# Kernel tuning notes

Measured on AMD Instinct MI355X. Metric: run time of the kernel, lower is better.

Reference implementation:

```python
import jax, jax.numpy as jnp
import numpy as np

BEV = 100  # fixed 100x100 BEV grid from __init__


def _bev_grids():
    # x: arange(-25+0.125, 25, 0.5) -> 100 vals; z: arange(0.125, 50, 0.5) -> 100 vals
    x = jnp.arange(-25.0 + 0.125, 25.0, 0.5, dtype=jnp.float32)
    z = jnp.arange(0.125, 50.0, 0.5, dtype=jnp.float32)
    zz, xx = jnp.meshgrid(z, x, indexing='ij')           # [100,100]
    xz = xx / zz                                          # [100,100]
    yz = jnp.stack([-1.0 / zz, 0.5 / zz, 2.0 / zz], 0)    # [3,100,100], planes y=-1,0.5,2
    return xz, yz


def _grid_sample_bilinear(img, grid):
    """torch.nn.functional.grid_sample, mode='bilinear', padding_mode='zeros',
    align_corners=False. img [B,C,H,W], grid [B,Hg,Wg,2] in [-1,1] (u=x, v=y)."""
    B, C, H, W = img.shape
    x = ((grid[..., 0] + 1.0) * W - 1.0) * 0.5            # unnormalized pixel x
    y = ((grid[..., 1] + 1.0) * H - 1.0) * 0.5
    x0f = jnp.floor(x)
    y0f = jnp.floor(y)
    x0 = x0f.astype(jnp.int32)
    y0 = y0f.astype(jnp.int32)
    x1 = x0 + 1
    y1 = y0 + 1
    wx1 = x - x0f
    wx0 = 1.0 - wx1
    wy1 = y - y0f
    wy0 = 1.0 - wy1

    def corner(xi, yi, w):
        valid = ((xi >= 0) & (xi < W) & (yi >= 0) & (yi < H)).astype(img.dtype)
        xi_c = jnp.clip(xi, 0, W - 1)
        yi_c = jnp.clip(yi, 0, H - 1)
        # per-batch gather: [C,H,W] indexed by [Hg,Wg] -> [C,Hg,Wg]
        vals = jax.vmap(lambda im, yy, xx_: im[:, yy, xx_])(img, yi_c, xi_c)
        return vals * (w * valid)[:, None]                 # [B,C,Hg,Wg]

    return (corner(x0, y0, wx0 * wy0) + corner(x1, y0, wx1 * wy0)
            + corner(x0, y1, wx0 * wy1) + corner(x1, y1, wx1 * wy1))


def setup_inputs() -> dict:
    key = jax.random.key(0)
    k1, k2, k3, k4, k5 = jax.random.split(key, 5)
    B, C, H, W = 8, 512, 88, 176
    img_w, img_h = 704, 352
    img_feature = jax.random.normal(k1, (B, C, H, W), dtype=jnp.float32)
    # realistic pinhole intrinsics so many BEV cells project in-bounds
    fx = jax.random.uniform(k2, (B,), minval=450.0, maxval=650.0)
    fy = jax.random.uniform(k3, (B,), minval=450.0, maxval=650.0)
    cx = img_w / 2.0 + jax.random.uniform(k4, (B,), minval=-8.0, maxval=8.0)
    cy = img_h / 2.0 + jax.random.uniform(k5, (B,), minval=-8.0, maxval=8.0)
    intrinsic = (jnp.zeros((B, 3, 3), dtype=jnp.float32)
                 .at[:, 0, 0].set(fx).at[:, 1, 1].set(fy)
                 .at[:, 0, 2].set(cx).at[:, 1, 2].set(cy)
                 .at[:, 2, 2].set(1.0))
    return {"img_feature": img_feature, "intrinsic": intrinsic,
            "img_w": img_w, "img_h": img_h}


def reference(img_feature, intrinsic, img_w, img_h):
    xz, yz = _bev_grids()
    fx = intrinsic[:, 0, 0][:, None, None]
    cx = intrinsic[:, 0, 2][:, None, None]
    fy = intrinsic[:, 1, 1][:, None, None]
    cy = intrinsic[:, 1, 2][:, None, None]
    u = ((fx * xz[None] + cx) / img_w - 0.5) * 2.0        # [B,100,100], shared by all 3 planes
    acc = None
    for k in range(3):                                     # 3 fixed height planes
        v = ((fy * yz[k][None] + cy) / img_h - 0.5) * 2.0
        grid = jnp.stack((u, v), axis=3)                   # [B,100,100,2]
        s = _grid_sample_bilinear(img_feature, grid)       # [B,C,100,100]
        acc = s if acc is None else acc + s
    return acc / 3.0
```

## Files before the change

### kernel.cpp

```cpp
#include <hip/hip_runtime.h>

#define BEVN 100
#define NB 8
#define NC 512
#define FH 88
#define FW 176
#define HWSZ (FH * FW)
#define NG4  (HWSZ / 4)
#define NPAIR (BEVN * BEVN / 2)

__device__ __forceinline__ unsigned bf16rne(float f) {
    const unsigned b = __float_as_uint(f);
    return (b + 0x7fffu + ((b >> 16) & 1u)) >> 16;
}
__device__ __forceinline__ float lo16f(unsigned u) { return __uint_as_float(u << 16); }
__device__ __forceinline__ float hi16f(unsigned u) { return __uint_as_float(u & 0xffff0000u); }

__global__ __launch_bounds__(1024, 8)
void vt_kernel(const float* __restrict__ img,
               const float* __restrict__ intr,
               const int* __restrict__ p_imw,
               const int* __restrict__ p_imh,
               float* __restrict__ out)
{
    __shared__ unsigned lds[HWSZ];
    __shared__ float4   ytab[BEVN * 3];

    const int blk = blockIdx.x;
    const int b   = blk >> 8;
    const int c0  = (blk & 255) * 2;
    const int bc0 = b * NC + c0;
    const int tid = (int)threadIdx.x;

    {
        const float4* __restrict__ s0 = (const float4*)(img + (size_t)bc0 * HWSZ);
        const float4* __restrict__ s1 = s0 + NG4;
        uint4* l4 = (uint4*)lds;
        for (int idx = tid; idx < NG4; idx += 1024) {
            const float4 a  = s0[idx];
            const float4 bb = s1[idx];
            uint4 u;
            u.x = bf16rne(a.x) | (bf16rne(bb.x) << 16);
            u.y = bf16rne(a.y) | (bf16rne(bb.y) << 16);
            u.z = bf16rne(a.z) | (bf16rne(bb.z) << 16);
            u.w = bf16rne(a.w) | (bf16rne(bb.w) << 16);
            l4[idx] = u;
        }
    }

    const float fx  = intr[b * 9 + 0];
    const float cxv = intr[b * 9 + 2];
    const float fy  = intr[b * 9 + 4];
    const float cyv = intr[b * 9 + 5];
    const float wsc = (float)FW / (float)p_imw[0];
    const float hsc = (float)FH / (float)p_imh[0];

    if (tid < BEVN * 3) {
        const int   i  = tid / 3;
        const int   k  = tid - 3 * i;
        const float z  = 0.125f + 0.5f * (float)i;
        const float iz = 1.0f / z;
        const float yk = (k == 0) ? -1.0f : ((k == 1) ? 0.5f : 2.0f);
        const float yp = fmaf(fy * yk * iz + cyv, hsc, -0.5f);
        const float yf = floorf(yp);
        const int   y0 = (int)yf;
        float wy1 = yp - yf;
        float wy0 = 1.0f - wy1;
        wy0 = ((unsigned)y0 < (unsigned)FH) ? wy0 : 0.0f;
        wy1 = ((unsigned)(y0 + 1) < (unsigned)FH) ? wy1 : 0.0f;
        const int yb0 = min(max(y0, 0), FH - 1) * FW;
        const int yb1 = min(max(y0 + 1, 0), FH - 1) * FW;
        float4 e;
        e.x = wy0 * (1.0f / 3.0f);
        e.y = wy1 * (1.0f / 3.0f);
        e.z = __int_as_float(yb0);
        e.w = __int_as_float(yb1);
        ytab[tid] = e;
    }

    __syncthreads();

    const float axs = 0.5f * fx * wsc;
    const float axb = -24.875f * fx * wsc;
    const float bx  = fmaf(cxv, wsc, -0.5f);

    float* __restrict__ op0 = out + (size_t)bc0 * (BEVN * BEVN);
    float* __restrict__ op1 = op0 + (BEVN * BEVN);

    for (int p = tid; p < NPAIR; p += 1024) {
        const int i  = p / 50;
        const int jp = p - 50 * i;
        const float z    = fmaf(0.5f, (float)i, 0.125f);
        const float invz = __builtin_amdgcn_rcpf(z);

        int   xb[2];
        float w0[2], w1[2];
        #pragma unroll
        for (int e = 0; e < 2; ++e) {
            const float aj   = fmaf((float)(2 * jp + e), axs, axb);
            const float xpix = fmaf(aj, invz, bx);
            const float f    = floorf(xpix);
            const int   x0   = (int)f;
            float wx1 = xpix - f;
            float wx0 = 1.0f - wx1;
            wx0 = ((unsigned)x0 < (unsigned)FW) ? wx0 : 0.0f;
            wx1 = ((unsigned)(x0 + 1) < (unsigned)FW) ? wx1 : 0.0f;
            const int xbe = min(max(x0, 0), FW - 2);
            const int d   = x0 - xbe;
            w0[e] = (d == 0) ? wx0 : ((d < 0) ? wx1 : 0.0f);
            w1[e] = (d == 0) ? wx1 : ((d < 0) ? 0.0f : wx0);
            xb[e] = xbe;
        }

        float2 rA, rB;
        const float wsum = (w0[0] + w1[0]) + (w0[1] + w1[1]);
        if (wsum == 0.0f) {
            rA.x = rA.y = rB.x = rB.y = 0.0f;
        } else {
            float accA[2] = {0.0f, 0.0f};
            float accB[2] = {0.0f, 0.0f};
            #pragma unroll
            for (int k = 0; k < 3; ++k) {
                const float4 e4  = ytab[i * 3 + k];
                const int    yb0 = __float_as_int(e4.z);
                const int    yb1 = __float_as_int(e4.w);
                #pragma unroll
                for (int e = 0; e < 2; ++e) {
                    const unsigned* r0 = lds + (yb0 + xb[e]);
                    const unsigned* r1 = lds + (yb1 + xb[e]);
                    const unsigned u00 = r0[0], u01 = r0[1];
                    const unsigned u10 = r1[0], u11 = r1[1];
                    const float h0a = fmaf(w1[e], lo16f(u01), w0[e] * lo16f(u00));
                    const float h1a = fmaf(w1[e], lo16f(u11), w0[e] * lo16f(u10));
                    accA[e] = fmaf(e4.x, h0a, accA[e]);
                    accA[e] = fmaf(e4.y, h1a, accA[e]);
                    const float h0b = fmaf(w1[e], hi16f(u01), w0[e] * hi16f(u00));
                    const float h1b = fmaf(w1[e], hi16f(u11), w0[e] * hi16f(u10));
                    accB[e] = fmaf(e4.x, h0b, accB[e]);
                    accB[e] = fmaf(e4.y, h1b, accB[e]);
                }
            }
            rA.x = accA[0]; rA.y = accA[1];
            rB.x = accB[0]; rB.y = accB[1];
        }
        *(float2*)(op0 + 2 * p) = rA;
        *(float2*)(op1 + 2 * p) = rB;
    }
}

extern "C" void kernel_launch(void* const* d_in, const int* in_sizes, int n_in,
                              void* d_out, int out_size, void* d_ws, size_t ws_size,
                              hipStream_t stream) {
    const float* img  = (const float*)d_in[0];
    const float* intr = (const float*)d_in[1];
    const int*   imw  = (const int*)d_in[2];
    const int*   imh  = (const int*)d_in[3];
    float*       out  = (float*)d_out;

    dim3 grid(NB * NC / 2);
    dim3 block(1024);
    hipLaunchKernelGGL(vt_kernel, grid, block, 0, stream,
                       img, intr, imw, imh, out);
}
```

Measured before the change: 91.26 us.

## Double-buffer LDS channel pairs with register prefetch across persistent blocks

```diff
diff --git a/kernel.cpp b/kernel.cpp
--- a/kernel.cpp
+++ b/kernel.cpp
@@ -8,6 +8,8 @@
 #define HWSZ (FH * FW)
 #define NG4  (HWSZ / 4)
 #define NPAIR (BEVN * BEVN / 2)
+#define NT   4
+#define NBLK (NB * NC / 2 / NT)
 
 __device__ __forceinline__ unsigned bf16rne(float f) {
     const unsigned b = __float_as_uint(f);
@@ -16,37 +18,20 @@
 __device__ __forceinline__ float lo16f(unsigned u) { return __uint_as_float(u << 16); }
 __device__ __forceinline__ float hi16f(unsigned u) { return __uint_as_float(u & 0xffff0000u); }
 
-__global__ __launch_bounds__(1024, 8)
+__global__ __launch_bounds__(1024, 4)
 void vt_kernel(const float* __restrict__ img,
                const float* __restrict__ intr,
                const int* __restrict__ p_imw,
                const int* __restrict__ p_imh,
                float* __restrict__ out)
 {
-    __shared__ unsigned lds[HWSZ];
+    __shared__ unsigned buf[2][HWSZ];
     __shared__ float4   ytab[BEVN * 3];
 
     const int blk = blockIdx.x;
-    const int b   = blk >> 8;
-    const int c0  = (blk & 255) * 2;
-    const int bc0 = b * NC + c0;
+    const int b   = blk >> 6;
+    const int cp0 = (blk & 63) * NT;
     const int tid = (int)threadIdx.x;
-
-    {
-        const float4* __restrict__ s0 = (const float4*)(img + (size_t)bc0 * HWSZ);
-        const float4* __restrict__ s1 = s0 + NG4;
-        uint4* l4 = (uint4*)lds;
-        for (int idx = tid; idx < NG4; idx += 1024) {
-            const float4 a  = s0[idx];
-            const float4 bb = s1[idx];
-            uint4 u;
-            u.x = bf16rne(a.x) | (bf16rne(bb.x) << 16);
-            u.y = bf16rne(a.y) | (bf16rne(bb.y) << 16);
-            u.z = bf16rne(a.z) | (bf16rne(bb.z) << 16);
-            u.w = bf16rne(a.w) | (bf16rne(bb.w) << 16);
-            l4[idx] = u;
-        }
-    }
 
     const float fx  = intr[b * 9 + 0];
     const float cxv = intr[b * 9 + 2];
@@ -78,73 +63,129 @@
         ytab[tid] = e;
     }
 
-    __syncthreads();
-
     const float axs = 0.5f * fx * wsc;
     const float axb = -24.875f * fx * wsc;
     const float bx  = fmaf(cxv, wsc, -0.5f);
 
-    float* __restrict__ op0 = out + (size_t)bc0 * (BEVN * BEVN);
-    float* __restrict__ op1 = op0 + (BEVN * BEVN);
-
-    for (int p = tid; p < NPAIR; p += 1024) {
-        const int i  = p / 50;
-        const int jp = p - 50 * i;
-        const float z    = fmaf(0.5f, (float)i, 0.125f);
-        const float invz = __builtin_amdgcn_rcpf(z);
-
-        int   xb[2];
-        float w0[2], w1[2];
+    float4 ra[4], rb[4];
+
+    {
+        const int bc0 = b * NC + 2 * cp0;
+        const float4* __restrict__ s0 = (const float4*)(img + (size_t)bc0 * HWSZ);
+        const float4* __restrict__ s1 = s0 + NG4;
+        uint4* l4 = (uint4*)buf[0];
         #pragma unroll
-        for (int e = 0; e < 2; ++e) {
-            const float aj   = fmaf((float)(2 * jp + e), axs, axb);
-            const float xpix = fmaf(aj, invz, bx);
-            const float f    = floorf(xpix);
-            const int   x0   = (int)f;
-            float wx1 = xpix - f;
-            float wx0 = 1.0f - wx1;
-            wx0 = ((unsigned)x0 < (unsigned)FW) ? wx0 : 0.0f;
-            wx1 = ((unsigned)(x0 + 1) < (unsigned)FW) ? wx1 : 0.0f;
-            const int xbe = min(max(x0, 0), FW - 2);
-            const int d   = x0 - xbe;
-            w0[e] = (d == 0) ? wx0 : ((d < 0) ? wx1 : 0.0f);
-            w1[e] = (d == 0) ? wx1 : ((d < 0) ? 0.0f : wx0);
-            xb[e] = xbe;
-        }
-
-        float2 rA, rB;
-        const float wsum = (w0[0] + w1[0]) + (w0[1] + w1[1]);
-        if (wsum == 0.0f) {
-            rA.x = rA.y = rB.x = rB.y = 0.0f;
-        } else {
-            float accA[2] = {0.0f, 0.0f};
-            float accB[2] = {0.0f, 0.0f};
+        for (int t = 0; t < 4; ++t) {
+            const int idx = tid + t * 1024;
+            if (idx < NG4) {
+                const float4 a  = s0[idx];
+                const float4 bb = s1[idx];
+                uint4 u;
+                u.x = bf16rne(a.x) | (bf16rne(bb.x) << 16);
+                u.y = bf16rne(a.y) | (bf16rne(bb.y) << 16);
+                u.z = bf16rne(a.z) | (bf16rne(bb.z) << 16);
+                u.w = bf16rne(a.w) | (bf16rne(bb.w) << 16);
+                l4[idx] = u;
+            }
+        }
+    }
+    __syncthreads();
+
+    for (int t = 0; t < NT; ++t) {
+        if (t + 1 < NT) {
+            const int bc0 = b * NC + 2 * (cp0 + t + 1);
+            const float4* __restrict__ s0 = (const float4*)(img + (size_t)bc0 * HWSZ);
+            const float4* __restrict__ s1 = s0 + NG4;
             #pragma unroll
-            for (int k = 0; k < 3; ++k) {
-                const float4 e4  = ytab[i * 3 + k];
-                const int    yb0 = __float_as_int(e4.z);
-                const int    yb1 = __float_as_int(e4.w);
+            for (int q = 0; q < 4; ++q) {
+                const int idx = tid + q * 1024;
+                if (idx < NG4) { ra[q] = s0[idx]; rb[q] = s1[idx]; }
+            }
+        }
+
+        {
+            const unsigned* __restrict__ cb = buf[t & 1];
+            const int bc0 = b * NC + 2 * (cp0 + t);
+            float* __restrict__ op0 = out + (size_t)bc0 * (BEVN * BEVN);
+            float* __restrict__ op1 = op0 + (BEVN * BEVN);
+
+            for (int p = tid; p < NPAIR; p += 1024) {
+                const int i  = p / 50;
+                const int jp = p - 50 * i;
+                const float z    = fmaf(0.5f, (float)i, 0.125f);
+                const float invz = __builtin_amdgcn_rcpf(z);
+
+                int   xb[2];
+                float w0[2], w1[2];
                 #pragma unroll
                 for (int e = 0; e < 2; ++e) {
-                    const unsigned* r0 = lds + (yb0 + xb[e]);
-                    const unsigned* r1 = lds + (yb1 + xb[e]);
-                    const unsigned u00 = r0[0], u01 = r0[1];
-                    const unsigned u10 = r1[0], u11 = r1[1];
-                    const float h0a = fmaf(w1[e], lo16f(u01), w0[e] * lo16f(u00));
-                    const float h1a = fmaf(w1[e], lo16f(u11), w0[e] * lo16f(u10));
-                    accA[e] = fmaf(e4.x, h0a, accA[e]);
-                    accA[e] = fmaf(e4.y, h1a, accA[e]);
-                    const float h0b = fmaf(w1[e], hi16f(u01), w0[e] * hi16f(u00));
-                    const float h1b = fmaf(w1[e], hi16f(u11), w0[e] * hi16f(u10));
-                    accB[e] = fmaf(e4.x, h0b, accB[e]);
-                    accB[e] = fmaf(e4.y, h1b, accB[e]);
+                    const float aj   = fmaf((float)(2 * jp + e), axs, axb);
+                    const float xpix = fmaf(aj, invz, bx);
+                    const float f    = floorf(xpix);
+                    const int   x0   = (int)f;
+                    float wx1 = xpix - f;
+                    float wx0 = 1.0f - wx1;
+                    wx0 = ((unsigned)x0 < (unsigned)FW) ? wx0 : 0.0f;
+                    wx1 = ((unsigned)(x0 + 1) < (unsigned)FW) ? wx1 : 0.0f;
+                    const int xbe = min(max(x0, 0), FW - 2);
+                    const int d   = x0 - xbe;
+                    w0[e] = (d == 0) ? wx0 : ((d < 0) ? wx1 : 0.0f);
+                    w1[e] = (d == 0) ? wx1 : ((d < 0) ? 0.0f : wx0);
+                    xb[e] = xbe;
                 }
-            }
-            rA.x = accA[0]; rA.y = accA[1];
-            rB.x = accB[0]; rB.y = accB[1];
-        }
-        *(float2*)(op0 + 2 * p) = rA;
-        *(float2*)(op1 + 2 * p) = rB;
+
+                float2 rA, rB;
+                const float wsum = (w0[0] + w1[0]) + (w0[1] + w1[1]);
+                if (wsum == 0.0f) {
+                    rA.x = rA.y = rB.x = rB.y = 0.0f;
+                } else {
+                    float accA[2] = {0.0f, 0.0f};
+                    float accB[2] = {0.0f, 0.0f};
+                    #pragma unroll
+                    for (int k = 0; k < 3; ++k) {
+                        const float4 e4  = ytab[i * 3 + k];
+                        const int    yb0 = __float_as_int(e4.z);
+                        const int    yb1 = __float_as_int(e4.w);
+                        #pragma unroll
+                        for (int e = 0; e < 2; ++e) {
+                            const unsigned* r0 = cb + (yb0 + xb[e]);
+                            const unsigned* r1 = cb + (yb1 + xb[e]);
+                            const unsigned u00 = r0[0], u01 = r0[1];
+                            const unsigned u10 = r1[0], u11 = r1[1];
+                            const float h0a = fmaf(w1[e], lo16f(u01), w0[e] * lo16f(u00));
+                            const float h1a = fmaf(w1[e], lo16f(u11), w0[e] * lo16f(u10));
+                            accA[e] = fmaf(e4.x, h0a, accA[e]);
+                            accA[e] = fmaf(e4.y, h1a, accA[e]);
+                            const float h0b = fmaf(w1[e], hi16f(u01), w0[e] * hi16f(u00));
+                            const float h1b = fmaf(w1[e], hi16f(u11), w0[e] * hi16f(u10));
+                            accB[e] = fmaf(e4.x, h0b, accB[e]);
+                            accB[e] = fmaf(e4.y, h1b, accB[e]);
+                        }
+                    }
+                    rA.x = accA[0]; rA.y = accA[1];
+                    rB.x = accB[0]; rB.y = accB[1];
+                }
+                *(float2*)(op0 + 2 * p) = rA;
+                *(float2*)(op1 + 2 * p) = rB;
+            }
+        }
+
+        if (t + 1 < NT) {
+            uint4* l4 = (uint4*)buf[(t + 1) & 1];
+            #pragma unroll
+            for (int q = 0; q < 4; ++q) {
+                const int idx = tid + q * 1024;
+                if (idx < NG4) {
+                    uint4 u;
+                    u.x = bf16rne(ra[q].x) | (bf16rne(rb[q].x) << 16);
+                    u.y = bf16rne(ra[q].y) | (bf16rne(rb[q].y) << 16);
+                    u.z = bf16rne(ra[q].z) | (bf16rne(rb[q].z) << 16);
+                    u.w = bf16rne(ra[q].w) | (bf16rne(rb[q].w) << 16);
+                    l4[idx] = u;
+                }
+            }
+        }
+        __syncthreads();
     }
 }
 
@@ -157,7 +198,7 @@
     const int*   imh  = (const int*)d_in[3];
     float*       out  = (float*)d_out;
 
-    dim3 grid(NB * NC / 2);
+    dim3 grid(NBLK);
     dim3 block(1024);
     hipLaunchKernelGGL(vt_kernel, grid, block, 0, stream,
                        img, intr, imw, imh, out);
```

Result: slower. 99.79 us (+9.3%).
